# Kernel tuning notes

Hardware: AMD Instinct MI355X
Metric: run time of the kernel (lower is better)

The kernel has to match this reference:

```python
import jax, jax.numpy as jnp
import numpy as np
from jax import lax

B, S, I, H, L = 128, 512, 128, 256, 2


def setup_inputs() -> dict:
    key = jax.random.key(0)
    ks = jax.random.split(key, 9)
    s_in = 1.0 / np.sqrt(I)
    s_h = 1.0 / np.sqrt(2 * H)
    return {
        "x": jax.random.normal(ks[0], (B, S, I), dtype=jnp.float32),
        "W_in": jax.random.normal(ks[1], (I, H), dtype=jnp.float32) * s_in,
        "b_in": jax.random.normal(ks[2], (H,), dtype=jnp.float32) * s_in,
        "Wz": jax.random.normal(ks[3], (L, 2 * H, H), dtype=jnp.float32) * s_h,
        "bz": jax.random.normal(ks[4], (L, H), dtype=jnp.float32) * s_h,
        "Wr": jax.random.normal(ks[5], (L, 2 * H, H), dtype=jnp.float32) * s_h,
        "br": jax.random.normal(ks[6], (L, H), dtype=jnp.float32) * s_h,
        "Wn": jax.random.normal(ks[7], (L, 2 * H, H), dtype=jnp.float32) * s_h,
        "bn": jax.random.normal(ks[8], (L, H), dtype=jnp.float32) * s_h,
    }


def reference(x, W_in, b_in, Wz, bz, Wr, br, Wn, bn):
    # x: [B, S, I] -> project to hidden once (matches self.input_layer(x))
    xp = jnp.einsum("bsi,ih->bsh", x, W_in) + b_in  # [B, S, H]
    n_layers = Wz.shape[0]
    b = x.shape[0]
    h0 = jnp.zeros((n_layers, b, H), dtype=x.dtype)

    def step(h, x_t):
        # h: [L, B, H], x_t: [B, H]
        inp = x_t
        h_next = []
        for l in range(n_layers):
            h_prev = h[l]
            comb = jnp.concatenate([inp, h_prev], axis=-1)  # [B, 2H]
            z = jax.nn.sigmoid(comb @ Wz[l] + bz[l])
            r = jax.nn.sigmoid(comb @ Wr[l] + br[l])
            comb2 = jnp.concatenate([inp, r * h_prev], axis=-1)
            n = jnp.tanh(comb2 @ Wn[l] + bn[l])
            hn = (1.0 - z) * n + z * h_prev
            h_next.append(hn)
            inp = hn
        h_new = jnp.stack(h_next)  # [L, B, H]
        return h_new, h_new[-1]

    h_final, outs = lax.scan(step, h0, jnp.swapaxes(xp, 0, 1))  # outs: [S, B, H]
    outputs = jnp.swapaxes(outs, 0, 1)  # [B, S, H]
    return outputs, h_final
```

## Files before the change

kernel.cpp:

```cpp
#include <hip/hip_runtime.h>
#include <stdint.h>

#define B_ 128
#define S_ 512
#define I_ 128
#define H_ 256

typedef short bf16x8 __attribute__((ext_vector_type(8)));
typedef short bf16x4 __attribute__((ext_vector_type(4)));
typedef float f32x4  __attribute__((ext_vector_type(4)));

__device__ __forceinline__ short f2bf(float f){
  unsigned u = __float_as_uint(f);
  u = (u + 0x7FFFu + ((u >> 16) & 1u)) >> 16;
  return (short)u;
}
__device__ __forceinline__ float bf2f(unsigned short u){
  return __uint_as_float(((unsigned)u) << 16);
}
__device__ __forceinline__ float sigmoidf_(float x){
  float e = __expf(-x);
  return __fdividef(1.f, 1.f + e);
}
__device__ __forceinline__ float tanhf_(float x){
  x = fminf(fmaxf(x, -10.f), 10.f);
  float e = __expf(2.f * x);
  return __fdividef(e - 1.f, e + 1.f);
}
__device__ __forceinline__ void bar_lds(){
  asm volatile("s_waitcnt lgkmcnt(0)" ::: "memory");
  __builtin_amdgcn_s_barrier();
}
#define MF(A, B, C) __builtin_amdgcn_mfma_f32_16x16x32_bf16((A), (B), (C), 0, 0, 0)

__global__ __launch_bounds__(256) void prep_compute(
    const float* __restrict__ W_in, const float* __restrict__ b_in,
    const float* __restrict__ Wz, const float* __restrict__ bz,
    const float* __restrict__ Wr, const float* __restrict__ br,
    const float* __restrict__ Wn, const float* __restrict__ bn,
    float* __restrict__ WcT, float* __restrict__ bc, float* __restrict__ bcat1)
{
  int id = blockIdx.x * 256 + threadIdx.x;
  if (id < 98304){
    int i = id / 768, gcol = id % 768;
    int g = gcol >> 8, n = gcol & 255;
    const float* Wg = (g == 0) ? Wz : (g == 1) ? Wr : Wn;
    float s = 0.f;
    for (int j = 0; j < 256; j++) s += W_in[i * 256 + j] * Wg[j * 256 + n];
    WcT[i * 768 + gcol] = s;
  } else if (id < 99072){
    int gcol = id - 98304;
    int g = gcol >> 8, n = gcol & 255;
    const float* Wg = (g == 0) ? Wz : (g == 1) ? Wr : Wn;
    const float* bg = (g == 0) ? bz : (g == 1) ? br : bn;
    float s = 0.f;
    for (int j = 0; j < 256; j++) s += b_in[j] * Wg[j * 256 + n];
    bc[gcol] = s + bg[n];
  } else if (id < 99840){
    int gcol = id - 99072;
    int g = gcol >> 8, n = gcol & 255;
    const float* bg = (g == 0) ? bz : (g == 1) ? br : bn;
    bcat1[gcol] = bg[256 + n];
  }
}

__global__ __launch_bounds__(256) void pack_wc(short* __restrict__ dst, const float* __restrict__ WcT)
{
  int id = blockIdx.x * 256 + threadIdx.x;
  int j = id & 7, l = (id >> 3) & 63, kt = (id >> 9) & 3, nt = id >> 11;
  int k = kt * 32 + (l >> 4) * 8 + j;
  int gcol = nt * 16 + (l & 15);
  dst[id] = f2bf(WcT[k * 768 + gcol]);
}

__global__ __launch_bounds__(256) void pack_top(short* __restrict__ dst,
    const float* __restrict__ Wz, const float* __restrict__ Wr, const float* __restrict__ Wn)
{
  int id = blockIdx.x * 256 + threadIdx.x;
  int j = id & 7, l = (id >> 3) & 63, kt = (id >> 9) & 7, nt = id >> 12;
  int k = kt * 32 + (l >> 4) * 8 + j;
  int gcol = nt * 16 + (l & 15);
  int g = gcol >> 8, n = gcol & 255;
  const float* W = (g == 0) ? Wz : (g == 1) ? Wr : Wn;
  dst[id] = f2bf(W[(size_t)(512 + k) * 256 + n]);
}

__global__ __launch_bounds__(256) void pack_zr(short* __restrict__ dst,
    const float* __restrict__ Wz, const float* __restrict__ Wr, int layer)
{
  int id = blockIdx.x * 256 + threadIdx.x;
  int j = id & 7, l = (id >> 3) & 63, kt = (id >> 9) & 7, nt = id >> 12;
  int k = kt * 32 + (l >> 4) * 8 + j;
  int n = (nt & 15) * 16 + (l & 15);
  const float* W = (nt < 16) ? Wz : Wr;
  dst[id] = f2bf(W[((size_t)layer * 512 + 256 + k) * 256 + n]);
}

__global__ __launch_bounds__(256) void pack_n(short* __restrict__ dst,
    const float* __restrict__ Wn, int layer)
{
  int id = blockIdx.x * 256 + threadIdx.x;
  int j = id & 7, l = (id >> 3) & 63, kt = (id >> 9) & 7, nt = id >> 12;
  int k = kt * 32 + (l >> 4) * 8 + j;
  int n = nt * 16 + (l & 15);
  dst[id] = f2bf(Wn[((size_t)layer * 512 + 256 + k) * 256 + n]);
}

__global__ __launch_bounds__(256) void gemm_g0(
    const float* __restrict__ Ap, const short* __restrict__ BF,
    const float* __restrict__ bias, short* __restrict__ C)
{
  const int tid = threadIdx.x, w = tid >> 6, l = tid & 63;
  const int m0 = blockIdx.x * 64 + w * 16;
  const int nb = blockIdx.y;
  const int K = 128;
  f32x4 zero4 = {0.f, 0.f, 0.f, 0.f};
  f32x4 acc[8];
#pragma unroll
  for (int nt = 0; nt < 8; nt++) acc[nt] = zero4;
#pragma unroll
  for (int kt = 0; kt < 4; kt++){
    const float* A = Ap + (size_t)(m0 + (l & 15)) * K + kt * 32 + (l >> 4) * 8;
    f32x4 a0 = *(const f32x4*)A;
    f32x4 a1 = *(const f32x4*)(A + 4);
    bf16x8 af;
    af[0] = f2bf(a0[0]); af[1] = f2bf(a0[1]); af[2] = f2bf(a0[2]); af[3] = f2bf(a0[3]);
    af[4] = f2bf(a1[0]); af[5] = f2bf(a1[1]); af[6] = f2bf(a1[2]); af[7] = f2bf(a1[3]);
#pragma unroll
    for (int nt = 0; nt < 8; nt++){
      bf16x8 bf = *(const bf16x8*)(BF + (size_t)(((nb * 8 + nt) * 4 + kt) * 64 + l) * 8);
      acc[nt] = MF(af, bf, acc[nt]);
    }
  }
#pragma unroll
  for (int nt = 0; nt < 8; nt++){
    int col = nb * 128 + nt * 16 + (l & 15);
    float bv = bias[col];
#pragma unroll
    for (int rr = 0; rr < 4; rr++){
      int mrow = m0 + (l >> 4) * 4 + rr;
      C[(size_t)mrow * 768 + col] = f2bf(acc[nt][rr] + bv);
    }
  }
}

__global__ __launch_bounds__(256) void repack6(const unsigned short* __restrict__ Gbuf,
                                               short* __restrict__ GpA4, unsigned* __restrict__ GpB2)
{
  int id = blockIdx.x * 256 + threadIdx.x;
  int cix = id & 15, wv = (id >> 4) & 7, t = (id >> 7) & 511, row = id >> 16;
  short v[6];
#pragma unroll
  for (int i = 0; i < 2; i++)
#pragma unroll
    for (int g = 0; g < 3; g++)
      v[i * 3 + g] =
        (short)Gbuf[((size_t)row * 512 + t) * 768 + g * 256 + i * 128 + wv * 16 + cix];
  bf16x4 a = {v[0], v[1], v[2], v[3]};
  *(bf16x4*)(GpA4 + (size_t)id * 4) = a;
  GpB2[id] = (unsigned)(unsigned short)v[4] | ((unsigned)(unsigned short)v[5] << 16);
}

__global__ __launch_bounds__(512, 1) void fused_recur(
    const short* __restrict__ GpA4, const unsigned* __restrict__ GpB2,
    const short* __restrict__ WZR0F, const short* __restrict__ WN0F,
    const short* __restrict__ WZR1F, const short* __restrict__ WN1F,
    const short* __restrict__ W1TF, const float* __restrict__ bcat1,
    short* __restrict__ pipe, float* __restrict__ out,
    float* __restrict__ finals, unsigned* __restrict__ flags)
{
  __shared__ __align__(16) char  ldsb[4096];
  __shared__ __align__(16) short p1L[12288];

  const int tid = threadIdx.x;
  const int w = tid >> 6, l = tid & 63;
  const int cix = l & 15, lk = l >> 4;
  const f32x4 Z4 = {0.f, 0.f, 0.f, 0.f};

  *(uint64_t*)(ldsb + tid * 8) = 0ull;

  const int A0 = (cix == 0) ? (lk << 4) : 1024;
  const int col0 = w * 16 + cix, col1 = col0 + 128;
  const int oA00 = col0 * 2, oA10 = col1 * 2;
  float h00 = 0.f, h10 = 0.f;

#define AF_ZR(KT) (*(const bf16x8*)(ldsb + A0 + (KT) * 64))
#define AF_N(KT)  (*(const bf16x8*)(ldsb + A0 + (KT) * 64 + 2048))

#define STEP_CORE(GATE_CODE, SINK_CODE) do { \
    bf16x8 x0 = AF_ZR(0), x1 = AF_ZR(1), x2 = AF_ZR(2), x3 = AF_ZR(3); \
    f32x4 az0 = Z4, az1 = Z4, ar0 = Z4, ar1 = Z4; \
    __builtin_amdgcn_s_setprio(1); \
    az0 = MF(x0, wzr[0][0], az0); az1 = MF(x0, wzr[1][0], az1); \
    ar0 = MF(x0, wzr[2][0], ar0); ar1 = MF(x0, wzr[3][0], ar1); x0 = AF_ZR(4); \
    az0 = MF(x1, wzr[0][1], az0); az1 = MF(x1, wzr[1][1], az1); \
    ar0 = MF(x1, wzr[2][1], ar0); ar1 = MF(x1, wzr[3][1], ar1); x1 = AF_ZR(5); \
    az0 = MF(x2, wzr[0][2], az0); az1 = MF(x2, wzr[1][2], az1); \
    ar0 = MF(x2, wzr[2][2], ar0); ar1 = MF(x2, wzr[3][2], ar1); x2 = AF_ZR(6); \
    az0 = MF(x3, wzr[0][3], az0); az1 = MF(x3, wzr[1][3], az1); \
    ar0 = MF(x3, wzr[2][3], ar0); ar1 = MF(x3, wzr[3][3], ar1); x3 = AF_ZR(7); \
    az0 = MF(x0, wzr[0][4], az0); az1 = MF(x0, wzr[1][4], az1); \
    ar0 = MF(x0, wzr[2][4], ar0); ar1 = MF(x0, wzr[3][4], ar1); \
    az0 = MF(x1, wzr[0][5], az0); az1 = MF(x1, wzr[1][5], az1); \
    ar0 = MF(x1, wzr[2][5], ar0); ar1 = MF(x1, wzr[3][5], ar1); \
    az0 = MF(x2, wzr[0][6], az0); az1 = MF(x2, wzr[1][6], az1); \
    ar0 = MF(x2, wzr[2][6], ar0); ar1 = MF(x2, wzr[3][6], ar1); \
    az0 = MF(x3, wzr[0][7], az0); az1 = MF(x3, wzr[1][7], az1); \
    ar0 = MF(x3, wzr[2][7], ar0); ar1 = MF(x3, wzr[3][7], ar1); \
    __builtin_amdgcn_s_setprio(0); \
    float gn00 = 0.f, gn10 = 0.f, zv00 = 0.f, zv10 = 0.f; \
    if (lk == 0){ \
      float gz00, gr00, gz10, gr10; \
      GATE_CODE \
      zv00 = sigmoidf_(az0[0] + gz00); zv10 = sigmoidf_(az1[0] + gz10); \
      float rv00 = sigmoidf_(ar0[0] + gr00), rv10 = sigmoidf_(ar1[0] + gr10); \
      *(short*)(ldsb + 2048 + oA00) = f2bf(rv00 * h00); \
      *(short*)(ldsb + 2048 + oA10) = f2bf(rv10 * h10); \
    } \
    bar_lds(); \
    bf16x8 y0 = AF_N(0), y1 = AF_N(1); \
    f32x4 an0 = Z4, an1 = Z4; \
    __builtin_amdgcn_s_setprio(1); \
    an0 = MF(y0, wn[0][0], an0); an1 = MF(y0, wn[1][0], an1); y0 = AF_N(2); \
    an0 = MF(y1, wn[0][1], an0); an1 = MF(y1, wn[1][1], an1); y1 = AF_N(3); \
    an0 = MF(y0, wn[0][2], an0); an1 = MF(y0, wn[1][2], an1); y0 = AF_N(4); \
    an0 = MF(y1, wn[0][3], an0); an1 = MF(y1, wn[1][3], an1); y1 = AF_N(5); \
    an0 = MF(y0, wn[0][4], an0); an1 = MF(y0, wn[1][4], an1); y0 = AF_N(6); \
    an0 = MF(y1, wn[0][5], an0); an1 = MF(y1, wn[1][5], an1); y1 = AF_N(7); \
    an0 = MF(y0, wn[0][6], an0); an1 = MF(y0, wn[1][6], an1); \
    an0 = MF(y1, wn[0][7], an0); an1 = MF(y1, wn[1][7], an1); \
    __builtin_amdgcn_s_setprio(0); \
    if (lk == 0){ \
      float nv00 = tanhf_(an0[0] + gn00), nv10 = tanhf_(an1[0] + gn10); \
      h00 = (1.f - zv00) * nv00 + zv00 * h00; \
      h10 = (1.f - zv10) * nv10 + zv10 * h10; \
      *(short*)(ldsb + oA00) = f2bf(h00); \
      *(short*)(ldsb + oA10) = f2bf(h10); \
      SINK_CODE \
    } \
    bar_lds(); \
  } while (0)

  if (blockIdx.x < 128){
    const int r0 = blockIdx.x;
    const int chunkBase = blockIdx.x * 65536 + w * 16 + cix;
    bf16x8 wzr[4][8], wn[2][8];
#pragma unroll
    for (int i = 0; i < 4; i++)
#pragma unroll
      for (int kt = 0; kt < 8; kt++)
        wzr[i][kt] = *(const bf16x8*)(WZR0F + (size_t)((((w + 8 * i) * 8 + kt) * 64 + l) * 8));
#pragma unroll
    for (int i = 0; i < 2; i++)
#pragma unroll
      for (int kt = 0; kt < 8; kt++)
        wn[i][kt] = *(const bf16x8*)(WN0F + (size_t)((((w + 8 * i) * 8 + kt) * 64 + l) * 8));
    __syncthreads();

    bf16x4 rgA0{}, rgA1{};
    unsigned rgB0 = 0, rgB1 = 0;
    if (lk == 0){
      rgA0 = *(const bf16x4*)(GpA4 + (size_t)chunkBase * 4);
      rgB0 = GpB2[chunkBase];
      rgA1 = *(const bf16x4*)(GpA4 + (size_t)(chunkBase + 128) * 4);
      rgB1 = GpB2[chunkBase + 128];
    }

#define GATE0(T, RGA, RGB) \
      gz00 = bf2f((unsigned short)RGA[0]); gr00 = bf2f((unsigned short)RGA[1]); \
      gn00 = bf2f((unsigned short)RGA[2]); \
      gz10 = bf2f((unsigned short)RGA[3]); \
      gr10 = bf2f((unsigned short)(RGB & 0xffffu)); \
      gn10 = bf2f((unsigned short)(RGB >> 16)); \
      { int tn = (T) + 2; if (tn >= S_) tn = (T); \
        size_t ch = (size_t)chunkBase + (size_t)tn * 128; \
        RGA = *(const bf16x4*)(GpA4 + ch * 4); \
        RGB = GpB2[ch]; }
#define SINK0(T) \
      { size_t ob = ((size_t)r0 * S_ + (T)) * H_; \
        pipe[ob + col0] = f2bf(h00); \
        pipe[ob + col1] = f2bf(h10); }

#pragma unroll 1
    for (int t = 0; t < S_; t += 2){
      STEP_CORE(GATE0(t, rgA0, rgB0), SINK0(t));
      STEP_CORE(GATE0(t + 1, rgA1, rgB1), SINK0(t + 1));
      if ((t & 15) == 14){
        __syncthreads();
        if (tid == 0)
          __hip_atomic_store(&flags[r0], (unsigned)((t + 2) >> 4),
                             __ATOMIC_RELEASE, __HIP_MEMORY_SCOPE_AGENT);
      }
    }
#undef GATE0
#undef SINK0
    if (lk == 0){
      finals[(size_t)r0 * H_ + col0] = h00;
      finals[(size_t)r0 * H_ + col1] = h10;
    }
  } else {
    const int b = blockIdx.x - 128;
    bf16x8 wzr[4][8], wn[2][8];
#pragma unroll
    for (int i = 0; i < 4; i++)
#pragma unroll
      for (int kt = 0; kt < 8; kt++)
        wzr[i][kt] = *(const bf16x8*)(WZR1F + (size_t)((((w + 8 * i) * 8 + kt) * 64 + l) * 8));
#pragma unroll
    for (int i = 0; i < 2; i++)
#pragma unroll
      for (int kt = 0; kt < 8; kt++)
        wn[i][kt] = *(const bf16x8*)(WN1F + (size_t)((((w + 8 * i) * 8 + kt) * 64 + l) * 8));
    __syncthreads();

    const short* wt0 = W1TF + (size_t)(w)      * 8 * 512 + l * 8;
    const short* wt1 = W1TF + (size_t)(16 + w) * 8 * 512 + l * 8;
    const short* wt2 = W1TF + (size_t)(32 + w) * 8 * 512 + l * 8;
    const short* wt3 = W1TF + (size_t)(8 + w)  * 8 * 512 + l * 8;
    const short* wt4 = W1TF + (size_t)(24 + w) * 8 * 512 + l * 8;
    const short* wt5 = W1TF + (size_t)(40 + w) * 8 * 512 + l * 8;
    float bb0 = bcat1[0 * 256 + 0 + w * 16 + cix];
    float bb1 = bcat1[1 * 256 + 0 + w * 16 + cix];
    float bb2 = bcat1[2 * 256 + 0 + w * 16 + cix];
    float bb3 = bcat1[0 * 256 + 128 + w * 16 + cix];
    float bb4 = bcat1[1 * 256 + 128 + w * 16 + cix];
    float bb5 = bcat1[2 * 256 + 128 + w * 16 + cix];
    short* p1Lw = p1L + w * 1536;

#pragma unroll 1
    for (int c = 0; c < 32; c++){
      if (tid == 0){
        unsigned target = (unsigned)(c + 1);
        int guard = 0;
        while (__hip_atomic_load(&flags[b], __ATOMIC_ACQUIRE, __HIP_MEMORY_SCOPE_AGENT) < target){
          __builtin_amdgcn_s_sleep(4);
          if (++guard > (1 << 20)) break;
        }
      }
      __syncthreads();

      const short* hp = pipe + ((size_t)b * 512 + c * 16 + cix) * 256 + lk * 8;
      f32x4 p0 = Z4, p1 = Z4, p2 = Z4, p3 = Z4, p4 = Z4, p5 = Z4;
      bf16x8 a0 = *(const bf16x8*)(hp + 0 * 32), a1 = *(const bf16x8*)(hp + 1 * 32);
      bf16x8 a2 = *(const bf16x8*)(hp + 2 * 32), a3 = *(const bf16x8*)(hp + 3 * 32);
      bf16x8 b0 = *(const bf16x8*)(wt0), b1 = *(const bf16x8*)(wt1), b2 = *(const bf16x8*)(wt2);
      bf16x8 b3 = *(const bf16x8*)(wt3), b4 = *(const bf16x8*)(wt4), b5 = *(const bf16x8*)(wt5);
#define GKT(AX, KTN) \
      p0 = MF(AX, b0, p0); b0 = *(const bf16x8*)(wt0 + (KTN) * 512); \
      p1 = MF(AX, b1, p1); b1 = *(const bf16x8*)(wt1 + (KTN) * 512); \
      p2 = MF(AX, b2, p2); b2 = *(const bf16x8*)(wt2 + (KTN) * 512); \
      p3 = MF(AX, b3, p3); b3 = *(const bf16x8*)(wt3 + (KTN) * 512); \
      p4 = MF(AX, b4, p4); b4 = *(const bf16x8*)(wt4 + (KTN) * 512); \
      p5 = MF(AX, b5, p5); b5 = *(const bf16x8*)(wt5 + (KTN) * 512);
#define GKTL(AX) \
      p0 = MF(AX, b0, p0); p1 = MF(AX, b1, p1); p2 = MF(AX, b2, p2); \
      p3 = MF(AX, b3, p3); p4 = MF(AX, b4, p4); p5 = MF(AX, b5, p5);
      GKT(a0, 1); a0 = *(const bf16x8*)(hp + 4 * 32);
      GKT(a1, 2); a1 = *(const bf16x8*)(hp + 5 * 32);
      GKT(a2, 3); a2 = *(const bf16x8*)(hp + 6 * 32);
      GKT(a3, 4); a3 = *(const bf16x8*)(hp + 7 * 32);
      GKT(a0, 5);
      GKT(a1, 6);
      GKT(a2, 7);
      GKTL(a3);
#undef GKT
#undef GKTL
#pragma unroll
      for (int r = 0; r < 4; r++){
        int tl = lk * 4 + r;
        int base = (tl * 16 + cix) * 6;
        unsigned u0 = (unsigned)(unsigned short)f2bf(p0[r]) | ((unsigned)(unsigned short)f2bf(p1[r]) << 16);
        unsigned u1 = (unsigned)(unsigned short)f2bf(p2[r]) | ((unsigned)(unsigned short)f2bf(p3[r]) << 16);
        unsigned u2 = (unsigned)(unsigned short)f2bf(p4[r]) | ((unsigned)(unsigned short)f2bf(p5[r]) << 16);
        *(unsigned*)(p1Lw + base)     = u0;
        *(unsigned*)(p1Lw + base + 2) = u1;
        *(unsigned*)(p1Lw + base + 4) = u2;
      }

#pragma unroll 1
      for (int ts = 0; ts < 16; ts++){
        int T = c * 16 + ts;
#define GATE1 \
        { const short* pb = p1Lw + (ts * 16 + cix) * 6; \
          unsigned u0 = *(const unsigned*)(pb); \
          unsigned u1 = *(const unsigned*)(pb + 2); \
          unsigned u2 = *(const unsigned*)(pb + 4); \
          gz00 = bf2f((unsigned short)(u0 & 0xffffu)) + bb0; \
          gr00 = bf2f((unsigned short)(u0 >> 16)) + bb1; \
          gn00 = bf2f((unsigned short)(u1 & 0xffffu)) + bb2; \
          gz10 = bf2f((unsigned short)(u1 >> 16)) + bb3; \
          gr10 = bf2f((unsigned short)(u2 & 0xffffu)) + bb4; \
          gn10 = bf2f((unsigned short)(u2 >> 16)) + bb5; }
#define SINK1 \
        { size_t ob = ((size_t)b * S_ + T) * H_; \
          out[ob + col0] = h00; \
          out[ob + col1] = h10; }
        STEP_CORE(GATE1, SINK1);
#undef GATE1
#undef SINK1
      }
    }
    if (lk == 0){
      finals[32768 + (size_t)b * H_ + col0] = h00;
      finals[32768 + (size_t)b * H_ + col1] = h10;
    }
  }
#undef STEP_CORE
#undef AF_ZR
#undef AF_N
}

extern "C" void kernel_launch(void* const* d_in, const int* in_sizes, int n_in,
                              void* d_out, int out_size, void* d_ws, size_t ws_size,
                              hipStream_t stream)
{
  (void)in_sizes; (void)n_in; (void)out_size; (void)ws_size;
  const float* x    = (const float*)d_in[0];
  const float* W_in = (const float*)d_in[1];
  const float* b_in = (const float*)d_in[2];
  const float* Wz   = (const float*)d_in[3];
  const float* bz   = (const float*)d_in[4];
  const float* Wr   = (const float*)d_in[5];
  const float* br   = (const float*)d_in[6];
  const float* Wn   = (const float*)d_in[7];
  const float* bn   = (const float*)d_in[8];
  float* out = (float*)d_out;

  char* ws = (char*)d_ws;
  short*    Gbuf  = (short*)(ws + 0);
  short*    GpA4  = (short*)(ws + 100663296);
  unsigned* GpB2  = (unsigned*)(ws + 167772160);
  float* WcT   = (float*)(ws + 201326592);
  float* bc    = (float*)(ws + 201719808);
  float* bcat1 = (float*)(ws + 201722880);
  short* WCF   = (short*)(ws + 201725952);
  short* W1TF  = (short*)(ws + 201922560);
  short* WZR0  = (short*)(ws + 202315776);
  short* WN0   = (short*)(ws + 202577920);
  short* WZR1  = (short*)(ws + 202708992);
  short* WN1   = (short*)(ws + 202971136);
  short* pipe  = (short*)(ws + 203102208);
  unsigned* flags = (unsigned*)(ws + 236656640);

  prep_compute<<<390, 256, 0, stream>>>(W_in, b_in, Wz, bz, Wr, br, Wn, bn, WcT, bc, bcat1);
  pack_wc <<<384, 256, 0, stream>>>(WCF, WcT);
  pack_top<<<768, 256, 0, stream>>>(W1TF, Wz, Wr, Wn);
  pack_zr <<<512, 256, 0, stream>>>(WZR0, Wz, Wr, 0);
  pack_n  <<<256, 256, 0, stream>>>(WN0, Wn, 0);
  pack_zr <<<512, 256, 0, stream>>>(WZR1, Wz, Wr, 1);
  pack_n  <<<256, 256, 0, stream>>>(WN1, Wn, 1);

  gemm_g0<<<dim3(1024, 6), 256, 0, stream>>>(x, WCF, bc, Gbuf);
  repack6<<<32768, 256, 0, stream>>>((const unsigned short*)Gbuf, GpA4, GpB2);
  hipMemsetAsync(flags, 0, 128 * sizeof(unsigned), stream);
  fused_recur<<<256, 512, 0, stream>>>(GpA4, GpB2, WZR0, WN0, WZR1, WN1, W1TF, bcat1,
                                       pipe, out, out + 16777216, flags);
}
```

Measured before the change: 1.361 ms.

## Move layer-1 input projection GEMM into layer-0 blocks via LDS-buffered hidden states

Layer-0 blocks now keep each 16-step chunk of hidden states in a swizzled LDS buffer. At the end of each chunk they run the layer-1 input-projection MFMA themselves, add the bias, and write packed bf16 gate inputs to global memory before raising the flag. Layer-1 blocks then only prefetch those packed gates, the same way layer 0 does, instead of running the chunk GEMM on their critical path. This rebalances work off the slower consumer and removes the bf16 hidden-state pipe buffer. The cost is extra compute and a __syncthreads on the producer once per chunk.

```diff
diff --git a/kernel.cpp b/kernel.cpp
--- a/kernel.cpp
+++ b/kernel.cpp
@@ -166,11 +166,12 @@
     const short* __restrict__ WZR0F, const short* __restrict__ WN0F,
     const short* __restrict__ WZR1F, const short* __restrict__ WN1F,
     const short* __restrict__ W1TF, const float* __restrict__ bcat1,
-    short* __restrict__ pipe, float* __restrict__ out,
-    float* __restrict__ finals, unsigned* __restrict__ flags)
+    short* __restrict__ P1A, unsigned* __restrict__ P1B,
+    float* __restrict__ out, float* __restrict__ finals,
+    unsigned* __restrict__ flags)
 {
   __shared__ __align__(16) char  ldsb[4096];
-  __shared__ __align__(16) short p1L[12288];
+  __shared__ __align__(16) short hC[4096];
 
   const int tid = threadIdx.x;
   const int w = tid >> 6, l = tid & 63;
@@ -241,9 +242,18 @@
     bar_lds(); \
   } while (0)
 
+#define GATE_RING(RGA, RGB, ARRA, ARRB, TN) \
+      gz00 = bf2f((unsigned short)RGA[0]); gr00 = bf2f((unsigned short)RGA[1]); \
+      gn00 = bf2f((unsigned short)RGA[2]); gz10 = bf2f((unsigned short)RGA[3]); \
+      gr10 = bf2f((unsigned short)(RGB & 0xffffu)); \
+      gn10 = bf2f((unsigned short)(RGB >> 16)); \
+      { size_t ch = (size_t)chunkBase + (size_t)(TN) * 128; \
+        RGA = *(const bf16x4*)(ARRA + ch * 4); \
+        RGB = ARRB[ch]; }
+
   if (blockIdx.x < 128){
     const int r0 = blockIdx.x;
-    const int chunkBase = blockIdx.x * 65536 + w * 16 + cix;
+    const int chunkBase = r0 * 65536 + w * 16 + cix;
     bf16x8 wzr[4][8], wn[2][8];
 #pragma unroll
     for (int i = 0; i < 4; i++)
@@ -256,6 +266,19 @@
       for (int kt = 0; kt < 8; kt++)
         wn[i][kt] = *(const bf16x8*)(WN0F + (size_t)((((w + 8 * i) * 8 + kt) * 64 + l) * 8));
     __syncthreads();
+
+    const short* wt0 = W1TF + (size_t)(w)      * 4096 + l * 8;
+    const short* wt1 = W1TF + (size_t)(16 + w) * 4096 + l * 8;
+    const short* wt2 = W1TF + (size_t)(32 + w) * 4096 + l * 8;
+    const short* wt3 = W1TF + (size_t)(8 + w)  * 4096 + l * 8;
+    const short* wt4 = W1TF + (size_t)(24 + w) * 4096 + l * 8;
+    const short* wt5 = W1TF + (size_t)(40 + w) * 4096 + l * 8;
+    const float bb0 = bcat1[0 * 256 + col0];
+    const float bb1 = bcat1[1 * 256 + col0];
+    const float bb2 = bcat1[2 * 256 + col0];
+    const float bb3 = bcat1[0 * 256 + col1];
+    const float bb4 = bcat1[1 * 256 + col1];
+    const float bb5 = bcat1[2 * 256 + col1];
 
     bf16x4 rgA0{}, rgA1{};
     unsigned rgB0 = 0, rgB1 = 0;
@@ -266,40 +289,61 @@
       rgB1 = GpB2[chunkBase + 128];
     }
 
-#define GATE0(T, RGA, RGB) \
-      gz00 = bf2f((unsigned short)RGA[0]); gr00 = bf2f((unsigned short)RGA[1]); \
-      gn00 = bf2f((unsigned short)RGA[2]); \
-      gz10 = bf2f((unsigned short)RGA[3]); \
-      gr10 = bf2f((unsigned short)(RGB & 0xffffu)); \
-      gn10 = bf2f((unsigned short)(RGB >> 16)); \
-      { int tn = (T) + 2; if (tn >= S_) tn = (T); \
-        size_t ch = (size_t)chunkBase + (size_t)tn * 128; \
-        RGA = *(const bf16x4*)(GpA4 + ch * 4); \
-        RGB = GpB2[ch]; }
-#define SINK0(T) \
-      { size_t ob = ((size_t)r0 * S_ + (T)) * H_; \
-        pipe[ob + col0] = f2bf(h00); \
-        pipe[ob + col1] = f2bf(h10); }
+#define SINK_HC(T) \
+      { int swz = ((T) & 7) << 4; int rowb = ((T) & 15) * 512; \
+        *(short*)((char*)hC + rowb + ((col0 * 2) ^ swz)) = f2bf(h00); \
+        *(short*)((char*)hC + rowb + ((col1 * 2) ^ swz)) = f2bf(h10); }
 
 #pragma unroll 1
-    for (int t = 0; t < S_; t += 2){
-      STEP_CORE(GATE0(t, rgA0, rgB0), SINK0(t));
-      STEP_CORE(GATE0(t + 1, rgA1, rgB1), SINK0(t + 1));
-      if ((t & 15) == 14){
-        __syncthreads();
-        if (tid == 0)
-          __hip_atomic_store(&flags[r0], (unsigned)((t + 2) >> 4),
-                             __ATOMIC_RELEASE, __HIP_MEMORY_SCOPE_AGENT);
+    for (int c = 0; c < 32; c++){
+#pragma unroll 1
+      for (int ts = 0; ts < 16; ts += 2){
+        int T = c * 16 + ts;
+        int tn0 = (T + 2 < S_) ? T + 2 : T;
+        int tn1 = (T + 3 < S_) ? T + 3 : T + 1;
+        STEP_CORE(GATE_RING(rgA0, rgB0, GpA4, GpB2, tn0), SINK_HC(T));
+        STEP_CORE(GATE_RING(rgA1, rgB1, GpA4, GpB2, tn1), SINK_HC(T + 1));
       }
-    }
-#undef GATE0
-#undef SINK0
+      {
+        f32x4 p0 = Z4, p1 = Z4, p2 = Z4, p3 = Z4, p4 = Z4, p5 = Z4;
+        bf16x8 b0 = *(const bf16x8*)(wt0), b1 = *(const bf16x8*)(wt1);
+        bf16x8 b2 = *(const bf16x8*)(wt2), b3 = *(const bf16x8*)(wt3);
+        bf16x8 b4 = *(const bf16x8*)(wt4), b5 = *(const bf16x8*)(wt5);
+#pragma unroll
+        for (int kt = 0; kt < 8; kt++){
+          bf16x8 a = *(const bf16x8*)((const char*)hC + cix * 512 +
+                                      ((kt * 64 + lk * 16) ^ ((cix & 7) << 4)));
+          p0 = MF(a, b0, p0); if (kt < 7) b0 = *(const bf16x8*)(wt0 + (kt + 1) * 512);
+          p1 = MF(a, b1, p1); if (kt < 7) b1 = *(const bf16x8*)(wt1 + (kt + 1) * 512);
+          p2 = MF(a, b2, p2); if (kt < 7) b2 = *(const bf16x8*)(wt2 + (kt + 1) * 512);
+          p3 = MF(a, b3, p3); if (kt < 7) b3 = *(const bf16x8*)(wt3 + (kt + 1) * 512);
+          p4 = MF(a, b4, p4); if (kt < 7) b4 = *(const bf16x8*)(wt4 + (kt + 1) * 512);
+          p5 = MF(a, b5, p5); if (kt < 7) b5 = *(const bf16x8*)(wt5 + (kt + 1) * 512);
+        }
+#pragma unroll
+        for (int rr = 0; rr < 4; rr++){
+          size_t id = (size_t)(r0 * 512 + c * 16 + lk * 4 + rr) * 128 + col0;
+          bf16x4 A;
+          A[0] = f2bf(p0[rr] + bb0); A[1] = f2bf(p1[rr] + bb1);
+          A[2] = f2bf(p2[rr] + bb2); A[3] = f2bf(p3[rr] + bb3);
+          *(bf16x4*)(P1A + id * 4) = A;
+          P1B[id] = (unsigned)(unsigned short)f2bf(p4[rr] + bb4) |
+                    ((unsigned)(unsigned short)f2bf(p5[rr] + bb5) << 16);
+        }
+      }
+      __syncthreads();
+      if (tid == 0)
+        __hip_atomic_store(&flags[r0], (unsigned)(c + 1),
+                           __ATOMIC_RELEASE, __HIP_MEMORY_SCOPE_AGENT);
+    }
+#undef SINK_HC
     if (lk == 0){
       finals[(size_t)r0 * H_ + col0] = h00;
       finals[(size_t)r0 * H_ + col1] = h10;
     }
   } else {
     const int b = blockIdx.x - 128;
+    const int chunkBase = b * 65536 + w * 16 + cix;
     bf16x8 wzr[4][8], wn[2][8];
 #pragma unroll
     for (int i = 0; i < 4; i++)
@@ -313,19 +357,10 @@
         wn[i][kt] = *(const bf16x8*)(WN1F + (size_t)((((w + 8 * i) * 8 + kt) * 64 + l) * 8));
     __syncthreads();
 
-    const short* wt0 = W1TF + (size_t)(w)      * 8 * 512 + l * 8;
-    const short* wt1 = W1TF + (size_t)(16 + w) * 8 * 512 + l * 8;
-    const short* wt2 = W1TF + (size_t)(32 + w) * 8 * 512 + l * 8;
-    const short* wt3 = W1TF + (size_t)(8 + w)  * 8 * 512 + l * 8;
-    const short* wt4 = W1TF + (size_t)(24 + w) * 8 * 512 + l * 8;
-    const short* wt5 = W1TF + (size_t)(40 + w) * 8 * 512 + l * 8;
-    float bb0 = bcat1[0 * 256 + 0 + w * 16 + cix];
-    float bb1 = bcat1[1 * 256 + 0 + w * 16 + cix];
-    float bb2 = bcat1[2 * 256 + 0 + w * 16 + cix];
-    float bb3 = bcat1[0 * 256 + 128 + w * 16 + cix];
-    float bb4 = bcat1[1 * 256 + 128 + w * 16 + cix];
-    float bb5 = bcat1[2 * 256 + 128 + w * 16 + cix];
-    short* p1Lw = p1L + w * 1536;
+#define SINK_OUT(T) \
+      { size_t ob = ((size_t)b * S_ + (T)) * H_; \
+        out[ob + col0] = h00; \
+        out[ob + col1] = h10; }
 
 #pragma unroll 1
     for (int c = 0; c < 32; c++){
@@ -339,73 +374,34 @@
       }
       __syncthreads();
 
-      const short* hp = pipe + ((size_t)b * 512 + c * 16 + cix) * 256 + lk * 8;
-      f32x4 p0 = Z4, p1 = Z4, p2 = Z4, p3 = Z4, p4 = Z4, p5 = Z4;
-      bf16x8 a0 = *(const bf16x8*)(hp + 0 * 32), a1 = *(const bf16x8*)(hp + 1 * 32);
-      bf16x8 a2 = *(const bf16x8*)(hp + 2 * 32), a3 = *(const bf16x8*)(hp + 3 * 32);
-      bf16x8 b0 = *(const bf16x8*)(wt0), b1 = *(const bf16x8*)(wt1), b2 = *(const bf16x8*)(wt2);
-      bf16x8 b3 = *(const bf16x8*)(wt3), b4 = *(const bf16x8*)(wt4), b5 = *(const bf16x8*)(wt5);
-#define GKT(AX, KTN) \
-      p0 = MF(AX, b0, p0); b0 = *(const bf16x8*)(wt0 + (KTN) * 512); \
-      p1 = MF(AX, b1, p1); b1 = *(const bf16x8*)(wt1 + (KTN) * 512); \
-      p2 = MF(AX, b2, p2); b2 = *(const bf16x8*)(wt2 + (KTN) * 512); \
-      p3 = MF(AX, b3, p3); b3 = *(const bf16x8*)(wt3 + (KTN) * 512); \
-      p4 = MF(AX, b4, p4); b4 = *(const bf16x8*)(wt4 + (KTN) * 512); \
-      p5 = MF(AX, b5, p5); b5 = *(const bf16x8*)(wt5 + (KTN) * 512);
-#define GKTL(AX) \
-      p0 = MF(AX, b0, p0); p1 = MF(AX, b1, p1); p2 = MF(AX, b2, p2); \
-      p3 = MF(AX, b3, p3); p4 = MF(AX, b4, p4); p5 = MF(AX, b5, p5);
-      GKT(a0, 1); a0 = *(const bf16x8*)(hp + 4 * 32);
-      GKT(a1, 2); a1 = *(const bf16x8*)(hp + 5 * 32);
-      GKT(a2, 3); a2 = *(const bf16x8*)(hp + 6 * 32);
-      GKT(a3, 4); a3 = *(const bf16x8*)(hp + 7 * 32);
-      GKT(a0, 5);
-      GKT(a1, 6);
-      GKT(a2, 7);
-      GKTL(a3);
-#undef GKT
-#undef GKTL
-#pragma unroll
-      for (int r = 0; r < 4; r++){
-        int tl = lk * 4 + r;
-        int base = (tl * 16 + cix) * 6;
-        unsigned u0 = (unsigned)(unsigned short)f2bf(p0[r]) | ((unsigned)(unsigned short)f2bf(p1[r]) << 16);
-        unsigned u1 = (unsigned)(unsigned short)f2bf(p2[r]) | ((unsigned)(unsigned short)f2bf(p3[r]) << 16);
-        unsigned u2 = (unsigned)(unsigned short)f2bf(p4[r]) | ((unsigned)(unsigned short)f2bf(p5[r]) << 16);
-        *(unsigned*)(p1Lw + base)     = u0;
-        *(unsigned*)(p1Lw + base + 2) = u1;
-        *(unsigned*)(p1Lw + base + 4) = u2;
+      bf16x4 rgA0{}, rgA1{};
+      unsigned rgB0 = 0, rgB1 = 0;
+      if (lk == 0){
+        size_t ch0 = (size_t)chunkBase + (size_t)(c * 16) * 128;
+        rgA0 = *(const bf16x4*)(P1A + ch0 * 4);
+        rgB0 = P1B[ch0];
+        rgA1 = *(const bf16x4*)(P1A + (ch0 + 128) * 4);
+        rgB1 = P1B[ch0 + 128];
       }
+      const int cend = c * 16 + 15;
 
 #pragma unroll 1
-      for (int ts = 0; ts < 16; ts++){
+      for (int ts = 0; ts < 16; ts += 2){
         int T = c * 16 + ts;
-#define GATE1 \
-        { const short* pb = p1Lw + (ts * 16 + cix) * 6; \
-          unsigned u0 = *(const unsigned*)(pb); \
-          unsigned u1 = *(const unsigned*)(pb + 2); \
-          unsigned u2 = *(const unsigned*)(pb + 4); \
-          gz00 = bf2f((unsigned short)(u0 & 0xffffu)) + bb0; \
-          gr00 = bf2f((unsigned short)(u0 >> 16)) + bb1; \
-          gn00 = bf2f((unsigned short)(u1 & 0xffffu)) + bb2; \
-          gz10 = bf2f((unsigned short)(u1 >> 16)) + bb3; \
-          gr10 = bf2f((unsigned short)(u2 & 0xffffu)) + bb4; \
-          gn10 = bf2f((unsigned short)(u2 >> 16)) + bb5; }
-#define SINK1 \
-        { size_t ob = ((size_t)b * S_ + T) * H_; \
-          out[ob + col0] = h00; \
-          out[ob + col1] = h10; }
-        STEP_CORE(GATE1, SINK1);
-#undef GATE1
-#undef SINK1
+        int tn0 = (T + 2 < cend) ? T + 2 : cend;
+        int tn1 = (T + 3 < cend) ? T + 3 : cend;
+        STEP_CORE(GATE_RING(rgA0, rgB0, P1A, P1B, tn0), SINK_OUT(T));
+        STEP_CORE(GATE_RING(rgA1, rgB1, P1A, P1B, tn1), SINK_OUT(T + 1));
       }
     }
+#undef SINK_OUT
     if (lk == 0){
       finals[32768 + (size_t)b * H_ + col0] = h00;
       finals[32768 + (size_t)b * H_ + col1] = h10;
     }
   }
 #undef STEP_CORE
+#undef GATE_RING
 #undef AF_ZR
 #undef AF_N
 }
@@ -428,6 +424,8 @@
 
   char* ws = (char*)d_ws;
   short*    Gbuf  = (short*)(ws + 0);
+  short*    P1A   = (short*)(ws + 0);
+  unsigned* P1B   = (unsigned*)(ws + 67108864);
   short*    GpA4  = (short*)(ws + 100663296);
   unsigned* GpB2  = (unsigned*)(ws + 167772160);
   float* WcT   = (float*)(ws + 201326592);
@@ -439,8 +437,7 @@
   short* WN0   = (short*)(ws + 202577920);
   short* WZR1  = (short*)(ws + 202708992);
   short* WN1   = (short*)(ws + 202971136);
-  short* pipe  = (short*)(ws + 203102208);
-  unsigned* flags = (unsigned*)(ws + 236656640);
+  unsigned* flags = (unsigned*)(ws + 203102208);
 
   prep_compute<<<390, 256, 0, stream>>>(W_in, b_in, Wz, bz, Wr, br, Wn, bn, WcT, bc, bcat1);
   pack_wc <<<384, 256, 0, stream>>>(WCF, WcT);
@@ -454,5 +451,5 @@
   repack6<<<32768, 256, 0, stream>>>((const unsigned short*)Gbuf, GpA4, GpB2);
   hipMemsetAsync(flags, 0, 128 * sizeof(unsigned), stream);
   fused_recur<<<256, 512, 0, stream>>>(GpA4, GpB2, WZR0, WN0, WZR1, WN1, W1TF, bcat1,
-                                       pipe, out, out + 16777216, flags);
-}
+                                       P1A, P1B, out, out + 16777216, flags);
+}
```

Result: slower. 2.687 ms (+97.4%).
